# Kernel tuning notes

Hardware: AMD Instinct MI355X
Metric: run time of the kernel (lower is better)

Reference implementation:

```python
import jax, jax.numpy as jnp
import numpy as np

N, C, K = 300000, 64, 27  # active voxels, channels, 3^3 kernel offsets


def sparse_conv(x, nbr, mask, W, b):
    """MinkowskiConvolution as gather -> GEMM -> accumulate.
    x: [N, C] features; nbr: [N, K] int32 neighbor index per kernel offset;
    mask: [N, K] bool validity; W: [K, C, C]; b: [C].
    out[i] = b + sum_k mask[i,k] * x[nbr[i,k]] @ W[k]
    Scans over the K=27 fixed kernel offsets so only an [N, C] gathered
    buffer is live at a time (never materializes [N, K, C]).
    """
    def step(acc, kin):
        Wk, nk, mk = kin
        g = jnp.where(mk[:, None], x[nk], jnp.zeros((), x.dtype))  # [N, C] gather
        return acc + g @ Wk, None

    acc0 = jnp.zeros_like(x) + b
    out, _ = jax.lax.scan(step, acc0, (W, nbr.T, mask.T))
    return out


def setup_inputs() -> dict:
    key = jax.random.key(0)
    ks = jax.random.split(key, 7)
    features = jax.random.normal(ks[0], (N, C), dtype=jnp.float32)
    neighbor_idx = jax.random.randint(ks[1], (N, K), 0, N, dtype=jnp.int32)
    neighbor_mask = jax.random.uniform(ks[2], (N, K)) < 0.6  # variable neighbor counts
    scale = 1.0 / np.sqrt(K * C)
    W0 = jax.random.normal(ks[3], (K, C, C), dtype=jnp.float32) * scale
    b0 = jax.random.normal(ks[4], (C,), dtype=jnp.float32) * 0.01
    W1 = jax.random.normal(ks[5], (K, C, C), dtype=jnp.float32) * scale
    b1 = jax.random.normal(ks[6], (C,), dtype=jnp.float32) * 0.01
    return {
        "features": features,
        "neighbor_idx": neighbor_idx,
        "neighbor_mask": neighbor_mask,
        "W0": W0, "b0": b0, "W1": W1, "b1": b1,
    }


def reference(features, neighbor_idx, neighbor_mask, W0, b0, W1, b1):
    # conv0 -> ReLU -> conv1 -> residual add (stride=1, shared kernel map)
    out = sparse_conv(features, neighbor_idx, neighbor_mask, W0, b0)
    out = jax.nn.relu(out)
    out = sparse_conv(out, neighbor_idx, neighbor_mask, W1, b1)
    return out + features
```

## Files before the change

### kernel.cpp

```cpp
#include <hip/hip_runtime.h>
#include <hip/hip_bf16.h>
#include <stdint.h>

typedef __bf16 bf16x8 __attribute__((ext_vector_type(8)));
typedef __bf16 bf16x4 __attribute__((ext_vector_type(4)));
typedef float f32x4 __attribute__((ext_vector_type(4)));
typedef unsigned short u16x4 __attribute__((ext_vector_type(4)));

__device__ __forceinline__ unsigned short f2bf(float f) {
    union { float f; uint32_t u; } v; v.f = f;
    uint32_t u = v.u;
    return (unsigned short)((u + 0x7fffu + ((u >> 16) & 1u)) >> 16);
}

__global__ __launch_bounds__(256) void prep_x(const f32x4* __restrict__ x,
                                              u16x4* __restrict__ xb, int n4, int n4tot) {
    int t = blockIdx.x * 256 + threadIdx.x;
    if (t < n4) {
        f32x4 v = x[t];
        u16x4 o;
        o.x = f2bf(v.x); o.y = f2bf(v.y); o.z = f2bf(v.z); o.w = f2bf(v.w);
        xb[t] = o;
    } else if (t < n4tot) {
        u16x4 z = {0, 0, 0, 0};
        xb[t] = z;
    }
}

__global__ void zero_row(unsigned short* __restrict__ p, long off) {
    p[off + threadIdx.x] = 0;
}

__global__ __launch_bounds__(256) void prep_w(const float* __restrict__ W,
                                              unsigned short* __restrict__ Wt, int K) {
    int k = blockIdx.x;
    unsigned short* Wtk = Wt + (size_t)k * 4352;
    const float* Wk = W + (size_t)k * 4096;
    for (int j = threadIdx.x; j < 4352; j += 256) {
        int co = j / 68, ci = j % 68;
        unsigned short v = 0;
        if (k < K && ci < 64) v = f2bf(Wk[ci * 64 + co]);
        Wtk[j] = v;
    }
}

__global__ void detect_mask(const unsigned int* __restrict__ m, int* __restrict__ flag) {
    __shared__ int s_not_int, s_not_f32;
    if (threadIdx.x == 0) { s_not_int = 0; s_not_f32 = 0; }
    __syncthreads();
    unsigned int w = m[threadIdx.x];
    if (w > 1u) s_not_int = 1;
    if (w != 0u && w != 0x3f800000u) s_not_f32 = 1;
    __syncthreads();
    if (threadIdx.x == 0) *flag = s_not_int ? (s_not_f32 ? 1 : 2) : 0;
}

template <int IOFF>
__device__ __forceinline__ bf16x8 gl16(const unsigned short* base, unsigned voff) {
    bf16x8 r;
    asm volatile("global_load_dwordx4 %0, %1, %2 offset:%c3"
                 : "=v"(r) : "v"(voff), "s"(base), "i"(IOFF));
    return r;
}

struct Slot { bf16x8 f[4]; };

template <int NW>
__device__ __forceinline__ void waitv(Slot& s) {
    asm volatile("s_waitcnt vmcnt(%c4)"
                 : "+v"(s.f[0]), "+v"(s.f[1]), "+v"(s.f[2]), "+v"(s.f[3])
                 : "i"(NW));
    __builtin_amdgcn_sched_barrier(0);
}

__device__ __forceinline__ void gload_lds16(const unsigned short* g, unsigned short* l) {
    __builtin_amdgcn_global_load_lds(
        (const __attribute__((address_space(1))) void*)(const void*)g,
        (__attribute__((address_space(3))) void*)(void*)l, 16, 0, 0);
}

__device__ __forceinline__ bf16x8 ldb(const unsigned short* p) {
    bf16x4 lo = *(const bf16x4*)p;
    bf16x4 hi = *(const bf16x4*)(p + 4);
    return __builtin_shufflevector(lo, hi, 0, 1, 2, 3, 4, 5, 6, 7);
}

template <int MODE>
__global__ __launch_bounds__(256, 2) void conv_mfma(
    const unsigned short* __restrict__ xb,
    const int* __restrict__ nbr,
    const void* __restrict__ maskp,
    const int* __restrict__ flagp,
    const unsigned short* __restrict__ Wt,
    const float* __restrict__ bias,
    const float* __restrict__ resid,
    void* __restrict__ outp,
    int N, int K)
{
    __shared__ unsigned short Wlds[2][17408];

    const int tid = threadIdx.x;
    const int wv  = tid >> 6;
    const int l   = tid & 63;
    const int lr  = l & 15;
    const int lg  = l >> 4;
    const int wavebase = blockIdx.x * 128 + wv * 32;

    const int myrow = wavebase + (l & 31);
    const int mr = myrow < N ? myrow : N - 1;

    unsigned mbits = 0;
    {
        const int flag = *flagp;
        long moff = (long)mr * K;
        if (flag == 1) {
            const unsigned char* mp = (const unsigned char*)maskp + moff;
#pragma unroll
            for (int k = 0; k < 27; ++k) mbits |= (mp[k] ? 1u : 0u) << k;
        } else if (flag == 0) {
            const int* mp = (const int*)maskp + moff;
#pragma unroll
            for (int k = 0; k < 27; ++k) mbits |= (mp[k] ? 1u : 0u) << k;
        } else {
            const float* mp = (const float*)maskp + moff;
#pragma unroll
            for (int k = 0; k < 27; ++k) mbits |= ((mp[k] != 0.f) ? 1u : 0u) << k;
        }
    }

    unsigned o[28];
    {
        const int* nrow = nbr + (long)mr * K;
#pragma unroll
        for (int k = 0; k < 27; ++k) {
            unsigned g = ((mbits >> k) & 1u) ? (unsigned)nrow[k] : (unsigned)N;
            o[k] = g * 128u;
        }
        o[27] = (unsigned)N * 128u;
    }

    const int bpa0 = ((l & 32) + lr) * 4;
    const int bpa1 = ((l & 32) + 16 + lr) * 4;
    const unsigned chk = (unsigned)(lg << 4);

    const int lr68 = lr * 68 + lg * 8;

    f32x4 acc[2][4] = {};
    Slot pipe[3];
    bf16x8 Bf[8];

#define STAGE(P) do { \
    const char* _srcb = (const char*)Wt + (size_t)(P) * 34816; \
    char* _dstb = (char*)(&Wlds[(P) & 1][0]); \
    _Pragma("unroll") \
    for (int _s = 0; _s < 9; ++_s) { \
        unsigned _off = (unsigned)(wv * 8704 + _s * 1024); \
        if (_off > 33792u) _off = 33792u; \
        gload_lds16((const unsigned short*)(_srcb + _off) + (l << 3), \
                    (unsigned short*)(_dstb + _off)); \
    } \
    asm volatile("" ::: "memory"); \
} while (0)

#define GISSUE(J) do { \
    unsigned _b0 = (unsigned)__builtin_amdgcn_ds_bpermute(bpa0, (int)o[J]) + chk; \
    unsigned _b1 = (unsigned)__builtin_amdgcn_ds_bpermute(bpa1, (int)o[J]) + chk; \
    Slot& _s = pipe[(J) % 3]; \
    _s.f[0] = gl16<0 >(xb, _b0); \
    _s.f[1] = gl16<64>(xb, _b0); \
    _s.f[2] = gl16<0 >(xb, _b1); \
    _s.f[3] = gl16<64>(xb, _b1); \
} while (0)

#define BLOAD(J) do { \
    const unsigned short* _wl = &Wlds[((J) >> 2) & 1][((J) & 3) * 4352]; \
    _Pragma("unroll") \
    for (int ct = 0; ct < 4; ++ct) { \
        const unsigned short* _wp = _wl + ct * 1088 + lr68; \
        Bf[ct * 2]     = ldb(_wp); \
        Bf[ct * 2 + 1] = ldb(_wp + 32); \
    } \
} while (0)

#define MFMA4(J) do { \
    Slot& _s = pipe[(J) % 3]; \
    _Pragma("unroll") \
    for (int ct = 0; ct < 4; ++ct) { \
        acc[0][ct] = __builtin_amdgcn_mfma_f32_16x16x32_bf16(_s.f[0], Bf[ct * 2],     acc[0][ct], 0, 0, 0); \
        acc[0][ct] = __builtin_amdgcn_mfma_f32_16x16x32_bf16(_s.f[1], Bf[ct * 2 + 1], acc[0][ct], 0, 0, 0); \
        acc[1][ct] = __builtin_amdgcn_mfma_f32_16x16x32_bf16(_s.f[2], Bf[ct * 2],     acc[1][ct], 0, 0, 0); \
        acc[1][ct] = __builtin_amdgcn_mfma_f32_16x16x32_bf16(_s.f[3], Bf[ct * 2 + 1], acc[1][ct], 0, 0, 0); \
    } \
} while (0)

#define FENCE() do { \
    __builtin_amdgcn_sched_barrier(0); \
    __builtin_amdgcn_s_barrier(); \
    __builtin_amdgcn_sched_barrier(0); \
} while (0)

#define STEP(J, NW) do { BLOAD(J); waitv<NW>(pipe[(J) % 3]); MFMA4(J); } while (0)

    STAGE(0);
    GISSUE(0); GISSUE(1);
    asm volatile("s_waitcnt vmcnt(8)" ::: "memory");
    __builtin_amdgcn_sched_barrier(0);
    __builtin_amdgcn_s_barrier();
    __builtin_amdgcn_sched_barrier(0);

    STAGE(1); GISSUE(2);  STEP(0, 17);
    GISSUE(3);  STEP(1, 17);
    GISSUE(4);  STEP(2, 8);
    GISSUE(5);  STEP(3, 8);
    FENCE();
    STAGE(2); GISSUE(6);  STEP(4, 17);
    GISSUE(7);  STEP(5, 17);
    GISSUE(8);  STEP(6, 8);
    GISSUE(9);  STEP(7, 8);
    FENCE();
    STAGE(3); GISSUE(10); STEP(8, 17);
    GISSUE(11); STEP(9, 17);
    GISSUE(12); STEP(10, 8);
    GISSUE(13); STEP(11, 8);
    FENCE();
    STAGE(4); GISSUE(14); STEP(12, 17);
    GISSUE(15); STEP(13, 17);
    GISSUE(16); STEP(14, 8);
    GISSUE(17); STEP(15, 8);
    FENCE();
    STAGE(5); GISSUE(18); STEP(16, 17);
    GISSUE(19); STEP(17, 17);
    GISSUE(20); STEP(18, 8);
    GISSUE(21); STEP(19, 8);
    FENCE();
    STAGE(6); GISSUE(22); STEP(20, 17);
    GISSUE(23); STEP(21, 17);
    GISSUE(24); STEP(22, 8);
    GISSUE(25); STEP(23, 8);
    FENCE();
    GISSUE(26); STEP(24, 8);
    GISSUE(27); STEP(25, 8);
    STEP(26, 4);
    STEP(27, 0);

#pragma unroll
    for (int at = 0; at < 2; ++at) {
#pragma unroll
        for (int ct = 0; ct < 4; ++ct) {
            int col = ct * 16 + lr;
            float bv = bias[col];
#pragma unroll
            for (int rg = 0; rg < 4; ++rg) {
                int row = wavebase + at * 16 + lg * 4 + rg;
                if (row < N) {
                    long oo = (long)row * 64 + col;
                    float v = acc[at][ct][rg] + bv;
                    if (MODE == 0) {
                        ((unsigned short*)outp)[oo] = f2bf(v > 0.f ? v : 0.f);
                    } else {
                        ((float*)outp)[oo] = v + resid[oo];
                    }
                }
            }
        }
    }

#undef STAGE
#undef GISSUE
#undef BLOAD
#undef MFMA4
#undef FENCE
#undef STEP
}

static inline size_t align256(size_t x) { return (x + 255) & ~(size_t)255; }

extern "C" void kernel_launch(void* const* d_in, const int* in_sizes, int n_in,
                              void* d_out, int out_size, void* d_ws, size_t ws_size,
                              hipStream_t stream) {
    const float* x    = (const float*)d_in[0];
    const int*   nbr  = (const int*)d_in[1];
    const void*  mask = d_in[2];
    const float* W0   = (const float*)d_in[3];
    const float* b0   = (const float*)d_in[4];
    const float* W1   = (const float*)d_in[5];
    const float* b1   = (const float*)d_in[6];

    const int NC = in_sizes[0];
    const int N  = NC / 64;
    const int K  = in_sizes[1] / N;
    const int KP = 28;

    char* ws = (char*)d_ws;
    size_t xb_bytes = (size_t)(NC + 64) * 2;
    size_t wt_bytes = (size_t)KP * 4352 * 2;
    size_t xb_off   = 0;
    size_t hb_off   = xb_off + align256(xb_bytes);
    size_t wt0_off  = hb_off + align256(xb_bytes);
    size_t wt1_off  = wt0_off + align256(wt_bytes);
    size_t flag_off = wt1_off + align256(wt_bytes);

    unsigned short* xb  = (unsigned short*)(ws + xb_off);
    unsigned short* hb  = (unsigned short*)(ws + hb_off);
    unsigned short* wt0 = (unsigned short*)(ws + wt0_off);
    unsigned short* wt1 = (unsigned short*)(ws + wt1_off);
    int* flag           = (int*)(ws + flag_off);

    int n4 = NC / 4;
    int n4tot = n4 + 16;
    prep_x<<<(n4tot + 255) / 256, 256, 0, stream>>>((const f32x4*)x, (u16x4*)xb, n4, n4tot);
    zero_row<<<1, 64, 0, stream>>>(hb, (long)NC);
    prep_w<<<KP, 256, 0, stream>>>(W0, wt0, K);
    prep_w<<<KP, 256, 0, stream>>>(W1, wt1, K);
    detect_mask<<<1, 1024, 0, stream>>>((const unsigned int*)mask, flag);

    int nblocks = (N + 127) / 128;
    conv_mfma<0><<<nblocks, 256, 0, stream>>>(xb, nbr, mask, flag, wt0, b0, nullptr, hb, N, K);
    conv_mfma<1><<<nblocks, 256, 0, stream>>>(hb, nbr, mask, flag, wt1, b1, x, d_out, N, K);
}
```

Measured before the change: 369.3 us.

## Widen each wave to 64 rows and pad weight rows for 16-byte LDS loads

Each wave now handles 64 output rows instead of 32, so every B fragment read from LDS feeds 16 MFMAs rather than 8, and each block covers 256 rows. The weight row stride is padded from 68 to 72 so B fragments load as single aligned 16-byte reads. The gather pipeline drops from three slots to two, with gathers issued after the matching MFMA step. This doubles accumulator and gather registers, which may lower occupancy, and the shallower pipeline may expose more gather latency.

```diff
diff --git a/kernel.cpp b/kernel.cpp
--- a/kernel.cpp
+++ b/kernel.cpp
@@ -3,7 +3,6 @@
 #include <stdint.h>
 
 typedef __bf16 bf16x8 __attribute__((ext_vector_type(8)));
-typedef __bf16 bf16x4 __attribute__((ext_vector_type(4)));
 typedef float f32x4 __attribute__((ext_vector_type(4)));
 typedef unsigned short u16x4 __attribute__((ext_vector_type(4)));
 
@@ -34,10 +33,10 @@
 __global__ __launch_bounds__(256) void prep_w(const float* __restrict__ W,
                                               unsigned short* __restrict__ Wt, int K) {
     int k = blockIdx.x;
-    unsigned short* Wtk = Wt + (size_t)k * 4352;
+    unsigned short* Wtk = Wt + (size_t)k * 4608;
     const float* Wk = W + (size_t)k * 4096;
-    for (int j = threadIdx.x; j < 4352; j += 256) {
-        int co = j / 68, ci = j % 68;
+    for (int j = threadIdx.x; j < 4608; j += 256) {
+        int co = j / 72, ci = j % 72;
         unsigned short v = 0;
         if (k < K && ci < 64) v = f2bf(Wk[ci * 64 + co]);
         Wtk[j] = v;
@@ -63,12 +62,13 @@
     return r;
 }
 
-struct Slot { bf16x8 f[4]; };
+struct Slot { bf16x8 f[8]; };
 
 template <int NW>
 __device__ __forceinline__ void waitv(Slot& s) {
-    asm volatile("s_waitcnt vmcnt(%c4)"
-                 : "+v"(s.f[0]), "+v"(s.f[1]), "+v"(s.f[2]), "+v"(s.f[3])
+    asm volatile("s_waitcnt vmcnt(%c8)"
+                 : "+v"(s.f[0]), "+v"(s.f[1]), "+v"(s.f[2]), "+v"(s.f[3]),
+                   "+v"(s.f[4]), "+v"(s.f[5]), "+v"(s.f[6]), "+v"(s.f[7])
                  : "i"(NW));
     __builtin_amdgcn_sched_barrier(0);
 }
@@ -77,12 +77,6 @@
     __builtin_amdgcn_global_load_lds(
         (const __attribute__((address_space(1))) void*)(const void*)g,
         (__attribute__((address_space(3))) void*)(void*)l, 16, 0, 0);
-}
-
-__device__ __forceinline__ bf16x8 ldb(const unsigned short* p) {
-    bf16x4 lo = *(const bf16x4*)p;
-    bf16x4 hi = *(const bf16x4*)(p + 4);
-    return __builtin_shufflevector(lo, hi, 0, 1, 2, 3, 4, 5, 6, 7);
 }
 
 template <int MODE>
@@ -97,16 +91,16 @@
     void* __restrict__ outp,
     int N, int K)
 {
-    __shared__ unsigned short Wlds[2][17408];
+    __shared__ unsigned short Wlds[2][18432];
 
     const int tid = threadIdx.x;
     const int wv  = tid >> 6;
     const int l   = tid & 63;
     const int lr  = l & 15;
     const int lg  = l >> 4;
-    const int wavebase = blockIdx.x * 128 + wv * 32;
-
-    const int myrow = wavebase + (l & 31);
+    const int wavebase = blockIdx.x * 256 + wv * 64;
+
+    const int myrow = wavebase + l;
     const int mr = myrow < N ? myrow : N - 1;
 
     unsigned mbits = 0;
@@ -139,112 +133,114 @@
         o[27] = (unsigned)N * 128u;
     }
 
-    const int bpa0 = ((l & 32) + lr) * 4;
-    const int bpa1 = ((l & 32) + 16 + lr) * 4;
+    const int bpa0 = (0 * 16 + lr) * 4;
+    const int bpa1 = (1 * 16 + lr) * 4;
+    const int bpa2 = (2 * 16 + lr) * 4;
+    const int bpa3 = (3 * 16 + lr) * 4;
     const unsigned chk = (unsigned)(lg << 4);
 
-    const int lr68 = lr * 68 + lg * 8;
-
-    f32x4 acc[2][4] = {};
-    Slot pipe[3];
+    const int lrw = lr * 72 + lg * 8;
+
+    f32x4 acc[4][4] = {};
+    Slot pipe[2];
     bf16x8 Bf[8];
 
 #define STAGE(P) do { \
-    const char* _srcb = (const char*)Wt + (size_t)(P) * 34816; \
-    char* _dstb = (char*)(&Wlds[(P) & 1][0]); \
+    const unsigned short* _src = Wt + (size_t)(P) * 18432 + wv * 4608 + (l << 3); \
+    unsigned short* _dst = &Wlds[(P) & 1][wv * 4608]; \
     _Pragma("unroll") \
-    for (int _s = 0; _s < 9; ++_s) { \
-        unsigned _off = (unsigned)(wv * 8704 + _s * 1024); \
-        if (_off > 33792u) _off = 33792u; \
-        gload_lds16((const unsigned short*)(_srcb + _off) + (l << 3), \
-                    (unsigned short*)(_dstb + _off)); \
-    } \
+    for (int _s = 0; _s < 9; ++_s) \
+        gload_lds16(_src + _s * 512, _dst + _s * 512); \
     asm volatile("" ::: "memory"); \
 } while (0)
 
 #define GISSUE(J) do { \
     unsigned _b0 = (unsigned)__builtin_amdgcn_ds_bpermute(bpa0, (int)o[J]) + chk; \
     unsigned _b1 = (unsigned)__builtin_amdgcn_ds_bpermute(bpa1, (int)o[J]) + chk; \
-    Slot& _s = pipe[(J) % 3]; \
-    _s.f[0] = gl16<0 >(xb, _b0); \
-    _s.f[1] = gl16<64>(xb, _b0); \
-    _s.f[2] = gl16<0 >(xb, _b1); \
-    _s.f[3] = gl16<64>(xb, _b1); \
+    unsigned _b2 = (unsigned)__builtin_amdgcn_ds_bpermute(bpa2, (int)o[J]) + chk; \
+    unsigned _b3 = (unsigned)__builtin_amdgcn_ds_bpermute(bpa3, (int)o[J]) + chk; \
+    Slot& _s = pipe[(J) & 1]; \
+    _s.f[0] = gl16<0 >(xb, _b0); _s.f[1] = gl16<64>(xb, _b0); \
+    _s.f[2] = gl16<0 >(xb, _b1); _s.f[3] = gl16<64>(xb, _b1); \
+    _s.f[4] = gl16<0 >(xb, _b2); _s.f[5] = gl16<64>(xb, _b2); \
+    _s.f[6] = gl16<0 >(xb, _b3); _s.f[7] = gl16<64>(xb, _b3); \
 } while (0)
 
 #define BLOAD(J) do { \
-    const unsigned short* _wl = &Wlds[((J) >> 2) & 1][((J) & 3) * 4352]; \
+    const unsigned short* _wl = &Wlds[((J) >> 2) & 1][((J) & 3) * 4608]; \
     _Pragma("unroll") \
     for (int ct = 0; ct < 4; ++ct) { \
-        const unsigned short* _wp = _wl + ct * 1088 + lr68; \
-        Bf[ct * 2]     = ldb(_wp); \
-        Bf[ct * 2 + 1] = ldb(_wp + 32); \
+        const unsigned short* _wp = _wl + ct * 1152 + lrw; \
+        Bf[ct * 2]     = *(const bf16x8*)(_wp); \
+        Bf[ct * 2 + 1] = *(const bf16x8*)(_wp + 32); \
     } \
 } while (0)
 
-#define MFMA4(J) do { \
-    Slot& _s = pipe[(J) % 3]; \
+#define MFMA16(J) do { \
+    Slot& _s = pipe[(J) & 1]; \
     _Pragma("unroll") \
     for (int ct = 0; ct < 4; ++ct) { \
-        acc[0][ct] = __builtin_amdgcn_mfma_f32_16x16x32_bf16(_s.f[0], Bf[ct * 2],     acc[0][ct], 0, 0, 0); \
-        acc[0][ct] = __builtin_amdgcn_mfma_f32_16x16x32_bf16(_s.f[1], Bf[ct * 2 + 1], acc[0][ct], 0, 0, 0); \
-        acc[1][ct] = __builtin_amdgcn_mfma_f32_16x16x32_bf16(_s.f[2], Bf[ct * 2],     acc[1][ct], 0, 0, 0); \
-        acc[1][ct] = __builtin_amdgcn_mfma_f32_16x16x32_bf16(_s.f[3], Bf[ct * 2 + 1], acc[1][ct], 0, 0, 0); \
+        _Pragma("unroll") \
+        for (int at = 0; at < 4; ++at) { \
+            acc[at][ct] = __builtin_amdgcn_mfma_f32_16x16x32_bf16(_s.f[at * 2],     Bf[ct * 2],     acc[at][ct], 0, 0, 0); \
+            acc[at][ct] = __builtin_amdgcn_mfma_f32_16x16x32_bf16(_s.f[at * 2 + 1], Bf[ct * 2 + 1], acc[at][ct], 0, 0, 0); \
+        } \
     } \
 } while (0)
 
 #define FENCE() do { \
+    asm volatile("s_waitcnt vmcnt(16)" ::: "memory"); \
     __builtin_amdgcn_sched_barrier(0); \
     __builtin_amdgcn_s_barrier(); \
     __builtin_amdgcn_sched_barrier(0); \
 } while (0)
 
-#define STEP(J, NW) do { BLOAD(J); waitv<NW>(pipe[(J) % 3]); MFMA4(J); } while (0)
+#define STEP(J, NW) do { BLOAD(J); waitv<NW>(pipe[(J) & 1]); MFMA16(J); } while (0)
 
     STAGE(0);
     GISSUE(0); GISSUE(1);
-    asm volatile("s_waitcnt vmcnt(8)" ::: "memory");
+    asm volatile("s_waitcnt vmcnt(16)" ::: "memory");
     __builtin_amdgcn_sched_barrier(0);
     __builtin_amdgcn_s_barrier();
     __builtin_amdgcn_sched_barrier(0);
 
-    STAGE(1); GISSUE(2);  STEP(0, 17);
-    GISSUE(3);  STEP(1, 17);
-    GISSUE(4);  STEP(2, 8);
-    GISSUE(5);  STEP(3, 8);
-    FENCE();
-    STAGE(2); GISSUE(6);  STEP(4, 17);
-    GISSUE(7);  STEP(5, 17);
-    GISSUE(8);  STEP(6, 8);
-    GISSUE(9);  STEP(7, 8);
-    FENCE();
-    STAGE(3); GISSUE(10); STEP(8, 17);
-    GISSUE(11); STEP(9, 17);
-    GISSUE(12); STEP(10, 8);
-    GISSUE(13); STEP(11, 8);
-    FENCE();
-    STAGE(4); GISSUE(14); STEP(12, 17);
-    GISSUE(15); STEP(13, 17);
-    GISSUE(16); STEP(14, 8);
-    GISSUE(17); STEP(15, 8);
-    FENCE();
-    STAGE(5); GISSUE(18); STEP(16, 17);
-    GISSUE(19); STEP(17, 17);
-    GISSUE(20); STEP(18, 8);
-    GISSUE(21); STEP(19, 8);
-    FENCE();
-    STAGE(6); GISSUE(22); STEP(20, 17);
-    GISSUE(23); STEP(21, 17);
-    GISSUE(24); STEP(22, 8);
-    GISSUE(25); STEP(23, 8);
-    FENCE();
-    GISSUE(26); STEP(24, 8);
-    GISSUE(27); STEP(25, 8);
-    STEP(26, 4);
+    STAGE(1); STEP(0, 17); GISSUE(2);
+    STEP(1, 17); GISSUE(3);
+    STEP(2, 8);  GISSUE(4);
+    STEP(3, 8);  GISSUE(5);
+    FENCE();
+    STAGE(2); STEP(4, 17); GISSUE(6);
+    STEP(5, 17); GISSUE(7);
+    STEP(6, 8);  GISSUE(8);
+    STEP(7, 8);  GISSUE(9);
+    FENCE();
+    STAGE(3); STEP(8, 17); GISSUE(10);
+    STEP(9, 17);  GISSUE(11);
+    STEP(10, 8);  GISSUE(12);
+    STEP(11, 8);  GISSUE(13);
+    FENCE();
+    STAGE(4); STEP(12, 17); GISSUE(14);
+    STEP(13, 17); GISSUE(15);
+    STEP(14, 8);  GISSUE(16);
+    STEP(15, 8);  GISSUE(17);
+    FENCE();
+    STAGE(5); STEP(16, 17); GISSUE(18);
+    STEP(17, 17); GISSUE(19);
+    STEP(18, 8);  GISSUE(20);
+    STEP(19, 8);  GISSUE(21);
+    FENCE();
+    STAGE(6); STEP(20, 17); GISSUE(22);
+    STEP(21, 17); GISSUE(23);
+    STEP(22, 8);  GISSUE(24);
+    STEP(23, 8);  GISSUE(25);
+    FENCE();
+    STEP(24, 8);  GISSUE(26);
+    STEP(25, 8);  GISSUE(27);
+    STEP(26, 8);
     STEP(27, 0);
 
 #pragma unroll
-    for (int at = 0; at < 2; ++at) {
+    for (int at = 0; at < 4; ++at) {
 #pragma unroll
         for (int ct = 0; ct < 4; ++ct) {
             int col = ct * 16 + lr;
@@ -268,7 +264,7 @@
 #undef STAGE
 #undef GISSUE
 #undef BLOAD
-#undef MFMA4
+#undef MFMA16
 #undef FENCE
 #undef STEP
 }
@@ -293,7 +289,7 @@
 
     char* ws = (char*)d_ws;
     size_t xb_bytes = (size_t)(NC + 64) * 2;
-    size_t wt_bytes = (size_t)KP * 4352 * 2;
+    size_t wt_bytes = (size_t)KP * 4608 * 2;
     size_t xb_off   = 0;
     size_t hb_off   = xb_off + align256(xb_bytes);
     size_t wt0_off  = hb_off + align256(xb_bytes);
@@ -314,7 +310,7 @@
     prep_w<<<KP, 256, 0, stream>>>(W1, wt1, K);
     detect_mask<<<1, 1024, 0, stream>>>((const unsigned int*)mask, flag);
 
-    int nblocks = (N + 127) / 128;
+    int nblocks = (N + 255) / 256;
     conv_mfma<0><<<nblocks, 256, 0, stream>>>(xb, nbr, mask, flag, wt0, b0, nullptr, hb, N, K);
     conv_mfma<1><<<nblocks, 256, 0, stream>>>(hb, nbr, mask, flag, wt1, b1, x, d_out, N, K);
 }
```

Result: faster. 357.3 us (-3.3%).
